# Optimization experiments

Hardware: AMD Instinct MI355X
Metric: run time of the kernel (lower is better)

## Reference

```python
import jax, jax.numpy as jnp
import numpy as np

B, DIM, H, W = 8, 384, 64, 64
HEADS = 8
D = DIM // HEADS          # 48
D2 = D // 2               # 24
DU = D // 3 * 2           # 32 (ratio=3)


def setup_inputs() -> dict:
    key = jax.random.key(0)
    ks = jax.random.split(key, 12)
    s = lambda k, shape, scale=0.05: jax.random.normal(k, shape, jnp.float32) * scale
    return {
        "x": jax.random.normal(ks[0], (B, DIM, H, W), jnp.float32),
        "temperature": jnp.ones((HEADS, 1, 1), jnp.float32),
        "w_qkv": s(ks[1], (3 * DIM, DIM)),          # 1x1 conv, no bias
        "w_dw": s(ks[2], (3 * DIM, 1, 3, 3)),       # depthwise 3x3, groups=3*dim
        "w_proj": s(ks[3], (DIM, HEADS)),           # project_out 1x1
        "w_attn_r": s(ks[4], (1, D)),
        "w_v_r": s(ks[5], (D2, D)),
        "w_up1": s(ks[6], (DU, D2)),
        "b_up1": jnp.zeros((DU,), jnp.float32),
        "ln_w": jnp.ones((DU, HEADS, 1), jnp.float32),
        "ln_b": jnp.zeros((DU, HEADS, 1), jnp.float32),
        "w_up2": s(ks[7], (D, DU)),
        "b_up2": jnp.zeros((D,), jnp.float32),
        "w_attn_l": s(ks[8], (D2, D)),
        "w_v_l": s(ks[9], (D2, D)),
    }


def _qkv_attn(x, temperature, w_qkv, w_dw):
    # shared: qkv 1x1 conv -> depthwise 3x3 -> split, normalize, elementwise attn+softmax
    b, c, h, w = x.shape
    qkv = jnp.einsum('bchw,oc->bohw', x, w_qkv)
    qkv = jax.lax.conv_general_dilated(
        qkv, w_dw, (1, 1), 'SAME', feature_group_count=3 * c,
        dimension_numbers=('NCHW', 'OIHW', 'NCHW'))
    q, k, v = jnp.split(qkv, 3, axis=1)
    rs = lambda t: t.reshape(b, HEADS, D, h * w)  # b (head d) h w -> b head d (hw)
    q, k, v = rs(q), rs(k), rs(v)
    qn = q / jnp.maximum(jnp.linalg.norm(q, axis=-1, keepdims=True), 1e-12)
    kn = k / jnp.maximum(jnp.linalg.norm(k, axis=-1, keepdims=True), 1e-12)
    attn = jax.nn.softmax(qn * kn * temperature, axis=-1)  # [b, head, d, s]
    return attn, v


def _forward(x, temperature, w_qkv, w_dw, w_proj, w_attn_r, w_v_r,
             w_up1, b_up1, ln_w, ln_b, w_up2, b_up2, w_attn_l, w_v_l):
    b, c, h, w = x.shape
    attn, v = _qkv_attn(x, temperature, w_qkv, w_dw)

    # ---- spatial_pool (channel gating) ----
    input_x = jnp.einsum('bhds,od->bhos', v, w_v_r)                 # conv_v_right: [b,head,d2,s]
    cm = jax.nn.softmax(jnp.einsum('bhds,d->bhs', attn, w_attn_r[0]), axis=-1)  # conv_attn_right + softmax
    ctx = jnp.einsum('bhs,bhjs->bhj', cm, input_x)                  # [b,head,d2]
    ctx = ctx.transpose(0, 2, 1)[..., None]                         # [b, d2, head, 1]
    u = jnp.einsum('bchl,oc->bohl', ctx, w_up1) + b_up1[None, :, None, None]  # [b, DU, head, 1]
    mu = u.mean(axis=(1, 2, 3), keepdims=True)
    var = u.var(axis=(1, 2, 3), keepdims=True)
    u = (u - mu) / jnp.sqrt(var + 1e-5) * ln_w[None] + ln_b[None]   # LayerNorm([DU, 8, 1])
    u = jax.nn.relu(u)
    u = jnp.einsum('bchl,oc->bohl', u, w_up2) + b_up2[None, :, None, None]    # [b, D, head, 1]
    mask_ch = jax.nn.sigmoid(u).reshape(b, c, 1, 1)                 # view(b, head*D, 1, 1)
    out_channel = x * mask_ch

    # ---- channel_pool (spatial gating) ----
    g = jnp.einsum('bhds,od->bhos', attn, w_attn_l)                 # conv_attn_left: [b,head,d2,s]
    avg = jax.nn.softmax(g.mean(axis=-1), axis=-1)                  # avg-pool over s, softmax over d2
    theta = jnp.einsum('bhds,od->bhos', v, w_v_l)                   # conv_v_left: [b,head,d2,s]
    ctx2 = jnp.einsum('bhd,bhds->bhs', avg, theta)                  # matmul: [b,head,s]
    mask_sp = jax.nn.sigmoid(ctx2).reshape(b, HEADS, h, w)
    mask_sp = jnp.einsum('bchw,oc->bohw', mask_sp, w_proj)          # project_out
    out_spatial = x * mask_sp

    return out_spatial + out_channel


def reference(x, temperature, w_qkv, w_dw, w_proj, w_attn_r, w_v_r,
              w_up1, b_up1, ln_w, ln_b, w_up2, b_up2, w_attn_l, w_v_l):
    return _forward(x, temperature, w_qkv, w_dw, w_proj, w_attn_r, w_v_r,
                    w_up1, b_up1, ln_w, ln_b, w_up2, b_up2, w_attn_l, w_v_l)
```

## Files before the change

### kernel.cpp

```cpp
#include <hip/hip_runtime.h>
#include <math.h>


#define S4096 4096
#define C384  384
#define OC    1152

typedef unsigned short bfraw;
typedef unsigned int   u32;
typedef __attribute__((ext_vector_type(8))) short bf16x8;
typedef __attribute__((ext_vector_type(4))) float f32x4;

typedef __attribute__((address_space(3))) unsigned int lds_u32;
typedef const __attribute__((address_space(1))) unsigned int glb_u32;
__device__ __forceinline__ void gll16(const void* g, void* l) {
    __builtin_amdgcn_global_load_lds((glb_u32*)g, (lds_u32*)l, 16, 0, 0);
}

__device__ __forceinline__ bfraw f2bf(float f) {
    union { float f; u32 u; } c; c.f = f;
    u32 r = c.u + 0x7FFFu + ((c.u >> 16) & 1u);
    return (bfraw)(r >> 16);
}
__device__ __forceinline__ float bf2f(bfraw u) {
    union { u32 u; float f; } c; c.u = ((u32)u) << 16;
    return c.f;
}
__device__ __forceinline__ void unpack8(uint4 v, float* f) {
    f[0] = bf2f((bfraw)(v.x & 0xffff)); f[1] = bf2f((bfraw)(v.x >> 16));
    f[2] = bf2f((bfraw)(v.y & 0xffff)); f[3] = bf2f((bfraw)(v.y >> 16));
    f[4] = bf2f((bfraw)(v.z & 0xffff)); f[5] = bf2f((bfraw)(v.z >> 16));
    f[6] = bf2f((bfraw)(v.w & 0xffff)); f[7] = bf2f((bfraw)(v.w >> 16));
}
__device__ __forceinline__ uint4 pack8(const float* f) {
    union { bfraw us[8]; uint4 q; } p;
    #pragma unroll
    for (int i = 0; i < 8; i++) p.us[i] = f2bf(f[i]);
    return p.q;
}

__device__ __forceinline__ float blk_red(float v, float* s4, bool ismax) {
    #pragma unroll
    for (int off = 32; off; off >>= 1) {
        float o = __shfl_down(v, off, 64);
        v = ismax ? fmaxf(v, o) : (v + o);
    }
    __syncthreads();
    if ((threadIdx.x & 63) == 0) s4[threadIdx.x >> 6] = v;
    __syncthreads();
    return ismax ? fmaxf(fmaxf(s4[0], s4[1]), fmaxf(s4[2], s4[3]))
                 : ((s4[0] + s4[1]) + (s4[2] + s4[3]));
}

__global__ void k0_prep(const float* __restrict__ w_attn_l,
                        const float* __restrict__ w_v_l,
                        float* __restrict__ weff) {
    __shared__ float avg[24];
    const int tid = threadIdx.x;
    if (tid < 24) {
        float a = 0.f;
        for (int d = 0; d < 48; d++) a += w_attn_l[tid * 48 + d];
        avg[tid] = a * (1.f / 4096.f);
    }
    __syncthreads();
    if (tid == 0) {
        float M = -3.402823466e+38f;
        for (int o = 0; o < 24; o++) M = fmaxf(M, avg[o]);
        float S = 0.f;
        for (int o = 0; o < 24; o++) { avg[o] = __expf(avg[o] - M); S += avg[o]; }
        float inv = 1.f / S;
        for (int o = 0; o < 24; o++) avg[o] *= inv;
    }
    __syncthreads();
    if (tid < 48) {
        float a = 0.f;
        for (int o = 0; o < 24; o++) a += avg[o] * w_v_l[o * 48 + tid];
        weff[tid] = a;
    }
}

__global__ __launch_bounds__(256) void kA_prep(
    const float* __restrict__ w_qkv, bfraw* __restrict__ wF) {
    const int id = blockIdx.x * 256 + threadIdx.x;
    const int ob = id / 768, rem = id % 768;
    const int c = rem / 48, kb = rem % 48;
    const float* src = w_qkv + (size_t)(ob * 16 + c) * C384 + kb * 8;
    float f[8];
    *(float4*)f       = *(const float4*)src;
    *(float4*)(f + 4) = *(const float4*)(src + 4);
    *(uint4*)&wF[((size_t)(ob * 48 + kb) * 16 + c) * 8] = pack8(f);
}

__global__ __launch_bounds__(256) void kB_tr(
    const float* __restrict__ x, bfraw* __restrict__ xF, int b0) {
    const int cb = blockIdx.x, sb = blockIdx.y, bl = blockIdx.z;
    const int c0 = cb * 16, s0 = sb * 256;
    const int tid = threadIdx.x;
    __shared__ alignas(16) bfraw lt[16][264];
    {
        const int r = tid >> 4, seg = tid & 15;
        const float* src = x + ((size_t)(b0 + bl) * C384 + c0 + r) * S4096 + s0 + seg * 16;
        float f[16];
        #pragma unroll
        for (int i = 0; i < 4; i++) *(float4*)(f + i * 4) = *(const float4*)(src + i * 4);
        *(uint4*)&lt[r][seg * 16]     = pack8(f);
        *(uint4*)&lt[r][seg * 16 + 8] = pack8(f + 8);
    }
    __syncthreads();
    const int sbl = tid >> 4, c = tid & 15;
    bfraw* xFb = xF + (size_t)bl * S4096 * C384;
    #pragma unroll
    for (int kbl = 0; kbl < 2; kbl++) {
        union { bfraw us[8]; uint4 q; } p;
        #pragma unroll
        for (int j = 0; j < 8; j++) p.us[j] = lt[kbl * 8 + j][sbl * 16 + c];
        const size_t idx = (((size_t)((s0 >> 4) + sbl) * 48) + (c0 >> 3) + kbl) * 128 + c * 8;
        *(uint4*)&xFb[idx] = p.q;
    }
}

__global__ __launch_bounds__(256) void k1_gemm(
    const bfraw* __restrict__ wF, const bfraw* __restrict__ xF,
    bfraw* __restrict__ pre, int b0) {
    __shared__ alignas(16) bfraw a_sm[4096];
    __shared__ alignas(16) bfraw b_sm[4096];
    const int tid = threadIdx.x;
    const int wave = tid >> 6, lane = tid & 63;
    const int sT = blockIdx.x, oT = blockIdx.y, bl = blockIdx.z;
    const bfraw* xFb = xF + (size_t)bl * S4096 * C384;

    f32x4 acc[4][4];
    #pragma unroll
    for (int m = 0; m < 4; m++)
        #pragma unroll
        for (int n = 0; n < 4; n++) acc[m][n] = (f32x4){0, 0, 0, 0};

    const int wr = (wave >> 1) * 4;
    const int wc = (wave & 1) * 4;

    for (int ks = 0; ks < 12; ks++) {
        const int kb0 = ks * 4;
        #pragma unroll
        for (int i = 0; i < 2; i++) {
            const int c = tid + i * 256;
            const int rb = c >> 6, oct = (c >> 4) & 3, row = c & 15;
            const bfraw* src = wF + ((size_t)((oT * 8 + rb) * 48 + kb0 + oct) * 16 + row) * 8;
            gll16(src, &a_sm[(size_t)c * 8]);
        }
        #pragma unroll
        for (int i = 0; i < 2; i++) {
            const int c = tid + i * 256;
            const int cb = c >> 6, oct = (c >> 4) & 3, col = c & 15;
            const bfraw* src = xFb + ((size_t)((sT * 8 + cb) * 48 + kb0 + oct) * 16 + col) * 8;
            gll16(src, &b_sm[(size_t)c * 8]);
        }
        __syncthreads();
        bf16x8 af[4], bq[4];
        #pragma unroll
        for (int m = 0; m < 4; m++) af[m] = *(const bf16x8*)&a_sm[((wr + m) * 64 + lane) * 8];
        #pragma unroll
        for (int n = 0; n < 4; n++) bq[n] = *(const bf16x8*)&b_sm[((wc + n) * 64 + lane) * 8];
        #pragma unroll
        for (int m = 0; m < 4; m++)
            #pragma unroll
            for (int n = 0; n < 4; n++)
                acc[m][n] = __builtin_amdgcn_mfma_f32_16x16x32_bf16(af[m], bq[n], acc[m][n], 0, 0, 0);
        __syncthreads();
    }
    bfraw* op = pre + (size_t)bl * OC * S4096;
    const int orow0 = oT * 128 + (wave >> 1) * 64 + (lane >> 4) * 4;
    const int scol0 = sT * 128 + (wave & 1) * 64 + (lane & 15);
    #pragma unroll
    for (int m = 0; m < 4; m++)
        #pragma unroll
        for (int n = 0; n < 4; n++)
            #pragma unroll
            for (int r = 0; r < 4; r++)
                op[(size_t)(orow0 + m * 16 + r) * S4096 + scol0 + n * 16] = f2bf(acc[m][n][r]);
}

__device__ __forceinline__ void stencil8(const bfraw* plane, const float* w9,
                                         int ypad, int k7, int x0, float* acc) {
    #pragma unroll
    for (int j = 0; j < 8; j++) acc[j] = 0.f;
    #pragma unroll
    for (int dy = 0; dy < 3; dy++) {
        uint4 rv = *(const uint4*)&plane[(ypad + dy) * 64 + x0];
        float r[8]; unpack8(rv, r);
        float lft = __shfl_up(r[7], 1);
        float rgt = __shfl_down(r[0], 1);
        if (k7 == 0) lft = 0.f;
        if (k7 == 7) rgt = 0.f;
        const float w0 = w9[dy*3], w1 = w9[dy*3+1], w2 = w9[dy*3+2];
        acc[0] += w0*lft + w1*r[0] + w2*r[1];
        #pragma unroll
        for (int j = 1; j < 7; j++) acc[j] += w0*r[j-1] + w1*r[j] + w2*r[j+1];
        acc[7] += w0*r[6] + w1*r[7] + w2*rgt;
    }
}

__global__ __launch_bounds__(256) void k2f(
    const bfraw* __restrict__ pre, const float* __restrict__ w_dw,
    const float* __restrict__ temperature,
    bfraw* __restrict__ av, int b0) {
    const int idx = blockIdx.x;
    const int bl  = blockIdx.y;
    const int h   = idx / 48;
    const int tid = threadIdx.x;
    __shared__ alignas(16) bfraw pl[3][66 * 64];
    __shared__ float s4[4];

    const size_t pbase = (size_t)bl * OC * S4096;
    #pragma unroll
    for (int p = 0; p < 3; p++) {
        const bfraw* src = pre + pbase + (size_t)(idx + p * C384) * S4096;
        uint4 a = *(const uint4*)&src[tid * 16];
        uint4 b = *(const uint4*)&src[tid * 16 + 8];
        int y = tid >> 2, xq = (tid & 3) * 16;
        *(uint4*)&pl[p][(y + 1) * 64 + xq]     = a;
        *(uint4*)&pl[p][(y + 1) * 64 + xq + 8] = b;
    }
    if (tid < 64) {
        #pragma unroll
        for (int p = 0; p < 3; p++) { pl[p][tid] = 0; pl[p][65 * 64 + tid] = 0; }
    }
    float wq[9], wk[9], wv[9];
    #pragma unroll
    for (int i = 0; i < 9; i++) {
        wq[i] = w_dw[idx * 9 + i];
        wk[i] = w_dw[(idx + C384) * 9 + i];
        wv[i] = w_dw[(idx + 768) * 9 + i];
    }
    __syncthreads();

    const int sid0 = tid,        y0 = sid0 >> 3, k70 = sid0 & 7, x00 = k70 * 8;
    const int sid1 = tid + 256,  y1 = sid1 >> 3, k71 = sid1 & 7, x01 = k71 * 8;
    float qo[16], ko[16], vo[16];
    stencil8(pl[0], wq, y0, k70, x00, qo);
    stencil8(pl[0], wq, y1, k71, x01, qo + 8);
    stencil8(pl[1], wk, y0, k70, x00, ko);
    stencil8(pl[1], wk, y1, k71, x01, ko + 8);
    stencil8(pl[2], wv, y0, k70, x00, vo);
    stencil8(pl[2], wv, y1, k71, x01, vo + 8);

    float sq = 0.f, sk = 0.f;
    #pragma unroll
    for (int i = 0; i < 16; i++) { sq += qo[i] * qo[i]; sk += ko[i] * ko[i]; }
    float Sq = blk_red(sq, s4, false);
    float Sk = blk_red(sk, s4, false);
    float scale = temperature[h] /
        (fmaxf(sqrtf(Sq), 1e-12f) * fmaxf(sqrtf(Sk), 1e-12f));
    float lm = -3.402823466e+38f;
    #pragma unroll
    for (int i = 0; i < 16; i++) { qo[i] = qo[i] * ko[i] * scale; lm = fmaxf(lm, qo[i]); }
    float M = blk_red(lm, s4, true);
    float ls = 0.f;
    #pragma unroll
    for (int i = 0; i < 16; i++) { qo[i] = __expf(qo[i] - M); ls += qo[i]; }
    float Z = blk_red(ls, s4, false);
    float invZ = 1.f / Z;
    #pragma unroll
    for (int i = 0; i < 16; i++) qo[i] *= invZ;

    bfraw* adst = av + ((size_t)bl * 768 + idx) * S4096;
    bfraw* vdst = av + ((size_t)bl * 768 + 384 + idx) * S4096;
    *(uint4*)&adst[y0 * 64 + x00] = pack8(qo);
    *(uint4*)&adst[y1 * 64 + x01] = pack8(qo + 8);
    *(uint4*)&vdst[y0 * 64 + x00] = pack8(vo);
    *(uint4*)&vdst[y1 * 64 + x01] = pack8(vo + 8);
}

__global__ __launch_bounds__(256) void k4a(
    const bfraw* __restrict__ av, const float* __restrict__ w_attn_r,
    const float* __restrict__ weff,
    float* __restrict__ cmraw, float* __restrict__ c2raw, int b0) {
    const int h = blockIdx.x, bl = blockIdx.y, st = blockIdx.z;
    const int b = b0 + bl;
    const int tid = threadIdx.x;
    __shared__ float swr[48], swf[48];
    if (tid < 48) { swr[tid] = w_attn_r[tid]; swf[tid] = weff[tid]; }
    __syncthreads();
    const int s_off = st * 1024 + tid * 4;
    const bfraw* abase = av + ((size_t)bl * 768 + h * 48) * S4096 + s_off;
    const bfraw* vbase = abase + (size_t)384 * S4096;
    float cmr[4] = {0,0,0,0}, c2[4] = {0,0,0,0};
    for (int d = 0; d < 48; d++) {
        uint2 ua = *(const uint2*)(abase + (size_t)d * S4096);
        uint2 uv = *(const uint2*)(vbase + (size_t)d * S4096);
        const float wr = swr[d], wf = swf[d];
        cmr[0] += bf2f((bfraw)(ua.x & 0xffff)) * wr;
        cmr[1] += bf2f((bfraw)(ua.x >> 16))    * wr;
        cmr[2] += bf2f((bfraw)(ua.y & 0xffff)) * wr;
        cmr[3] += bf2f((bfraw)(ua.y >> 16))    * wr;
        c2[0]  += bf2f((bfraw)(uv.x & 0xffff)) * wf;
        c2[1]  += bf2f((bfraw)(uv.x >> 16))    * wf;
        c2[2]  += bf2f((bfraw)(uv.y & 0xffff)) * wf;
        c2[3]  += bf2f((bfraw)(uv.y >> 16))    * wf;
    }
    const size_t o = ((size_t)(b * 8 + h)) * S4096 + s_off;
    float4 a4 = {cmr[0], cmr[1], cmr[2], cmr[3]};
    float4 b4 = {c2[0], c2[1], c2[2], c2[3]};
    *(float4*)(cmraw + o) = a4;
    *(float4*)(c2raw + o) = b4;
}

__global__ __launch_bounds__(256) void k4b(
    const float* __restrict__ cmraw, const float* __restrict__ c2raw,
    bfraw* __restrict__ cmb, float* __restrict__ msp, int b0) {
    const int h = blockIdx.x, bl = blockIdx.y, b = b0 + bl;
    const int tid = threadIdx.x;
    __shared__ float s4[4];
    const size_t base = ((size_t)(b * 8 + h)) * S4096 + tid * 16;
    float v[16];
    #pragma unroll
    for (int i = 0; i < 4; i++) *(float4*)(v + i * 4) = *(const float4*)(cmraw + base + i * 4);
    float lm = -3.402823466e+38f;
    #pragma unroll
    for (int i = 0; i < 16; i++) lm = fmaxf(lm, v[i]);
    float M = blk_red(lm, s4, true);
    float ls = 0.f;
    #pragma unroll
    for (int i = 0; i < 16; i++) { v[i] = __expf(v[i] - M); ls += v[i]; }
    float Z = blk_red(ls, s4, false);
    float inv = 1.f / Z;
    #pragma unroll
    for (int i = 0; i < 16; i++) v[i] *= inv;
    *(uint4*)(cmb + base)     = pack8(v);
    *(uint4*)(cmb + base + 8) = pack8(v + 8);
    #pragma unroll
    for (int i = 0; i < 4; i++) {
        float4 c = *(const float4*)(c2raw + base + i * 4);
        float4 m;
        m.x = 1.f / (1.f + __expf(-c.x)); m.y = 1.f / (1.f + __expf(-c.y));
        m.z = 1.f / (1.f + __expf(-c.z)); m.w = 1.f / (1.f + __expf(-c.w));
        *(float4*)(msp + base + i * 4) = m;
    }
}

__global__ __launch_bounds__(256) void k5_vc(
    const bfraw* __restrict__ av, const bfraw* __restrict__ cmb,
    float* __restrict__ vc, int b0) {
    const int idx = blockIdx.x;
    const int bl = blockIdx.y, b = b0 + bl;
    const int h = idx / 48;
    const int tid = threadIdx.x;
    const bfraw* vr = av + ((size_t)bl * 768 + 384 + idx) * S4096 + tid * 16;
    const bfraw* cr = cmb + ((size_t)(b * 8 + h)) * S4096 + tid * 16;
    float vv[16], cc[16];
    { uint4 a = *(const uint4*)vr, c = *(const uint4*)(vr + 8); unpack8(a, vv); unpack8(c, vv + 8); }
    { uint4 a = *(const uint4*)cr, c = *(const uint4*)(cr + 8); unpack8(a, cc); unpack8(c, cc + 8); }
    float a = 0.f;
    #pragma unroll
    for (int i = 0; i < 16; i++) a += vv[i] * cc[i];
    __shared__ float s4[4];
    float S = blk_red(a, s4, false);
    if (tid == 0) vc[b * C384 + idx] = S;
}

__global__ __launch_bounds__(256) void k6_gate(
    const float* __restrict__ vc, const float* __restrict__ w_v_r,
    const float* __restrict__ w_up1, const float* __restrict__ b_up1,
    const float* __restrict__ ln_w, const float* __restrict__ ln_b,
    const float* __restrict__ w_up2, const float* __restrict__ b_up2,
    float* __restrict__ mch, int b0) {
    const int b = b0 + blockIdx.x;
    const int tid = threadIdx.x;
    __shared__ float s_vc[384], s_ctx[192], s_u[256], s4[4];
    for (int i = tid; i < 384; i += 256) s_vc[i] = vc[b * C384 + i];
    __syncthreads();
    if (tid < 192) {
        int hh = tid / 24, o = tid % 24;
        float a = 0.f;
        for (int d = 0; d < 48; d++) a += w_v_r[o * 48 + d] * s_vc[hh * 48 + d];
        s_ctx[hh * 24 + o] = a;
    }
    __syncthreads();
    float uval;
    {
        int o = tid >> 3, hh = tid & 7;
        float a = b_up1[o];
        for (int c = 0; c < 24; c++) a += w_up1[o * 24 + c] * s_ctx[hh * 24 + c];
        uval = a;
    }
    float mu  = blk_red(uval, s4, false) * (1.f / 256.f);
    float dv  = uval - mu;
    float var = blk_red(dv * dv, s4, false) * (1.f / 256.f);
    float un  = dv * rsqrtf(var + 1e-5f) * ln_w[tid] + ln_b[tid];
    s_u[tid] = fmaxf(un, 0.f);
    __syncthreads();
    for (int t = tid; t < 384; t += 256) {
        int o2 = t >> 3, hh = t & 7;
        float a = b_up2[o2];
        for (int o = 0; o < 32; o++) a += w_up2[o2 * 32 + o] * s_u[o * 8 + hh];
        mch[b * C384 + t] = 1.f / (1.f + __expf(-a));
    }
}

__global__ __launch_bounds__(256) void k7_out(
    const float* __restrict__ x, const float* __restrict__ w_proj,
    const float* __restrict__ mch, const float* __restrict__ msp,
    float* __restrict__ out, int b0) {
    const int st = blockIdx.x, cg = blockIdx.y, bl = blockIdx.z;
    const int b = b0 + bl;
    const int tid = threadIdx.x;
    const int s0 = st * 256, c0 = cg * 48;
    __shared__ float s_msp[8][256];
    __shared__ float s_mch[48];
    __shared__ float s_wp[48][8];
    for (int i = tid; i < 2048; i += 256) {
        int hh = i >> 8, ss = i & 255;
        s_msp[hh][ss] = msp[((size_t)(b * 8 + hh)) * S4096 + s0 + ss];
    }
    if (tid < 48) s_mch[tid] = mch[b * C384 + c0 + tid];
    for (int i = tid; i < 384; i += 256)
        s_wp[i >> 3][i & 7] = w_proj[(size_t)(c0 + (i >> 3)) * 8 + (i & 7)];
    __syncthreads();

    const int cl = tid >> 6;
    const int s4i = (tid & 63) * 4;
    float4 m[8];
    #pragma unroll
    for (int hh = 0; hh < 8; hh++) m[hh] = *(const float4*)&s_msp[hh][s4i];

    #pragma unroll 4
    for (int j = 0; j < 12; j++) {
        const int cloc = j * 4 + cl;
        const int c = c0 + cloc;
        const float base = s_mch[cloc];
        float4 a = {base, base, base, base};
        #pragma unroll
        for (int hh = 0; hh < 8; hh++) {
            const float wp = s_wp[cloc][hh];
            a.x += wp * m[hh].x; a.y += wp * m[hh].y;
            a.z += wp * m[hh].z; a.w += wp * m[hh].w;
        }
        const size_t o = ((size_t)b * C384 + c) * S4096 + s0 + s4i;
        float4 xv = *(const float4*)(x + o);
        a.x *= xv.x; a.y *= xv.y; a.z *= xv.z; a.w *= xv.w;
        *(float4*)(out + o) = a;
    }
}

extern "C" void kernel_launch(void* const* d_in, const int* in_sizes, int n_in,
                              void* d_out, int out_size, void* d_ws, size_t ws_size,
                              hipStream_t stream) {
    const float* x        = (const float*)d_in[0];
    const float* temp     = (const float*)d_in[1];
    const float* w_qkv    = (const float*)d_in[2];
    const float* w_dw     = (const float*)d_in[3];
    const float* w_proj   = (const float*)d_in[4];
    const float* w_attn_r = (const float*)d_in[5];
    const float* w_v_r    = (const float*)d_in[6];
    const float* w_up1    = (const float*)d_in[7];
    const float* b_up1    = (const float*)d_in[8];
    const float* ln_w     = (const float*)d_in[9];
    const float* ln_b     = (const float*)d_in[10];
    const float* w_up2    = (const float*)d_in[11];
    const float* b_up2    = (const float*)d_in[12];
    const float* w_attn_l = (const float*)d_in[13];
    const float* w_v_l    = (const float*)d_in[14];
    float* out = (float*)d_out;
    char* ws = (char*)d_ws;

    size_t off = 0;
    auto alloc = [&](size_t bytes) {
        size_t o = off; off = (off + bytes + 255) & ~(size_t)255; return o;
    };
    float* cmraw = (float*)(ws + alloc((size_t)64 * S4096 * 4));
    float* c2raw = (float*)(ws + alloc((size_t)64 * S4096 * 4));
    bfraw* cmb   = (bfraw*)(ws + alloc((size_t)64 * S4096 * 2));
    float* msp   = (float*)(ws + alloc((size_t)64 * S4096 * 4));
    float* vc    = (float*)(ws + alloc(3072 * 4));
    float* mch   = (float*)(ws + alloc(3072 * 4));
    float* weff  = (float*)(ws + alloc(256));
    bfraw* wF    = (bfraw*)(ws + alloc((size_t)55296 * 16));
    const size_t big_xF  = (size_t)S4096 * C384 * 2;
    const size_t big_pre = (size_t)OC * S4096 * 2;
    const size_t big_av  = (size_t)768 * S4096 * 2;
    int nb = (ws_size >= off + 8 * (big_xF + big_pre + big_av)) ? 8 : 1;
    bfraw* xF  = (bfraw*)(ws + alloc((size_t)nb * big_xF));
    bfraw* pre = (bfraw*)(ws + alloc((size_t)nb * big_pre));
    bfraw* av  = (bfraw*)(ws + alloc((size_t)nb * big_av));

    k0_prep<<<1, 64, 0, stream>>>(w_attn_l, w_v_l, weff);
    kA_prep<<<216, 256, 0, stream>>>(w_qkv, wF);
    for (int b0 = 0; b0 < 8; b0 += nb) {
        kB_tr<<<dim3(24, 16, nb), 256, 0, stream>>>(x, xF, b0);
        k1_gemm<<<dim3(32, 9, nb), 256, 0, stream>>>(wF, xF, pre, b0);
        k2f<<<dim3(384, nb), 256, 0, stream>>>(pre, w_dw, temp, av, b0);
        k4a<<<dim3(8, nb, 4), 256, 0, stream>>>(av, w_attn_r, weff, cmraw, c2raw, b0);
        k4b<<<dim3(8, nb), 256, 0, stream>>>(cmraw, c2raw, cmb, msp, b0);
        k5_vc<<<dim3(384, nb), 256, 0, stream>>>(av, cmb, vc, b0);
        k6_gate<<<dim3(nb), 256, 0, stream>>>(vc, w_v_r, w_up1, b_up1,
                                              ln_w, ln_b, w_up2, b_up2, mch, b0);
        k7_out<<<dim3(16, 8, nb), 256, 0, stream>>>(x, w_proj, mch, msp, out, b0);
    }
}
```

Baseline: 130.4 us.

## Double-buffer GEMM LDS loads, stage epilogue through LDS, merge prep kernels

The QKV GEMM now double-buffers its LDS tiles, issuing the global-to-LDS loads for the next K step before running the MFMAs on the current one. The epilogue writes the bf16 tile into padded LDS and then stores 16-byte vectors per row instead of scattered 2-byte stores. The tiny weff prep kernel is folded into kA_prep as an extra block, saving one launch. The larger LDS footprint (about 34 KB per block) may cut occupancy.

```diff
diff --git a/kernel.cpp b/kernel.cpp
--- a/kernel.cpp
+++ b/kernel.cpp
@@ -52,35 +52,35 @@
                  : ((s4[0] + s4[1]) + (s4[2] + s4[3]));
 }
 
-__global__ void k0_prep(const float* __restrict__ w_attn_l,
-                        const float* __restrict__ w_v_l,
-                        float* __restrict__ weff) {
-    __shared__ float avg[24];
-    const int tid = threadIdx.x;
-    if (tid < 24) {
-        float a = 0.f;
-        for (int d = 0; d < 48; d++) a += w_attn_l[tid * 48 + d];
-        avg[tid] = a * (1.f / 4096.f);
-    }
-    __syncthreads();
-    if (tid == 0) {
-        float M = -3.402823466e+38f;
-        for (int o = 0; o < 24; o++) M = fmaxf(M, avg[o]);
-        float S = 0.f;
-        for (int o = 0; o < 24; o++) { avg[o] = __expf(avg[o] - M); S += avg[o]; }
-        float inv = 1.f / S;
-        for (int o = 0; o < 24; o++) avg[o] *= inv;
-    }
-    __syncthreads();
-    if (tid < 48) {
-        float a = 0.f;
-        for (int o = 0; o < 24; o++) a += avg[o] * w_v_l[o * 48 + tid];
-        weff[tid] = a;
-    }
-}
-
 __global__ __launch_bounds__(256) void kA_prep(
-    const float* __restrict__ w_qkv, bfraw* __restrict__ wF) {
+    const float* __restrict__ w_qkv, bfraw* __restrict__ wF,
+    const float* __restrict__ w_attn_l, const float* __restrict__ w_v_l,
+    float* __restrict__ weff) {
+    if (blockIdx.x == 216) {
+        __shared__ float avg[24];
+        const int tid = threadIdx.x;
+        if (tid < 24) {
+            float a = 0.f;
+            for (int d = 0; d < 48; d++) a += w_attn_l[tid * 48 + d];
+            avg[tid] = a * (1.f / 4096.f);
+        }
+        __syncthreads();
+        if (tid == 0) {
+            float M = -3.402823466e+38f;
+            for (int o = 0; o < 24; o++) M = fmaxf(M, avg[o]);
+            float S = 0.f;
+            for (int o = 0; o < 24; o++) { avg[o] = __expf(avg[o] - M); S += avg[o]; }
+            float inv = 1.f / S;
+            for (int o = 0; o < 24; o++) avg[o] *= inv;
+        }
+        __syncthreads();
+        if (tid < 48) {
+            float a = 0.f;
+            for (int o = 0; o < 24; o++) a += avg[o] * w_v_l[o * 48 + tid];
+            weff[tid] = a;
+        }
+        return;
+    }
     const int id = blockIdx.x * 256 + threadIdx.x;
     const int ob = id / 768, rem = id % 768;
     const int c = rem / 48, kb = rem % 48;
@@ -122,13 +122,16 @@
 __global__ __launch_bounds__(256) void k1_gemm(
     const bfraw* __restrict__ wF, const bfraw* __restrict__ xF,
     bfraw* __restrict__ pre, int b0) {
-    __shared__ alignas(16) bfraw a_sm[4096];
-    __shared__ alignas(16) bfraw b_sm[4096];
+    __shared__ alignas(16) bfraw smem[17408];
     const int tid = threadIdx.x;
     const int wave = tid >> 6, lane = tid & 63;
     const int sT = blockIdx.x, oT = blockIdx.y, bl = blockIdx.z;
     const bfraw* xFb = xF + (size_t)bl * S4096 * C384;
 
+    const int c0_ = tid, c1_ = tid + 256;
+    const int rb0 = c0_ >> 6, oc0 = (c0_ >> 4) & 3, rw0 = c0_ & 15;
+    const int rb1 = c1_ >> 6, oc1 = (c1_ >> 4) & 3, rw1 = c1_ & 15;
+
     f32x4 acc[4][4];
     #pragma unroll
     for (int m = 0; m < 4; m++)
@@ -138,28 +141,30 @@
     const int wr = (wave >> 1) * 4;
     const int wc = (wave & 1) * 4;
 
+    auto stage = [&](bfraw* dst, int kb0) {
+        gll16(wF  + ((size_t)((oT * 8 + rb0) * 48 + kb0 + oc0) * 16 + rw0) * 8,
+              dst + (size_t)c0_ * 8);
+        gll16(wF  + ((size_t)((oT * 8 + rb1) * 48 + kb0 + oc1) * 16 + rw1) * 8,
+              dst + (size_t)c1_ * 8);
+        gll16(xFb + ((size_t)((sT * 8 + rb0) * 48 + kb0 + oc0) * 16 + rw0) * 8,
+              dst + 4096 + (size_t)c0_ * 8);
+        gll16(xFb + ((size_t)((sT * 8 + rb1) * 48 + kb0 + oc1) * 16 + rw1) * 8,
+              dst + 4096 + (size_t)c1_ * 8);
+    };
+
+    stage(smem, 0);
+    __syncthreads();
+
     for (int ks = 0; ks < 12; ks++) {
-        const int kb0 = ks * 4;
-        #pragma unroll
-        for (int i = 0; i < 2; i++) {
-            const int c = tid + i * 256;
-            const int rb = c >> 6, oct = (c >> 4) & 3, row = c & 15;
-            const bfraw* src = wF + ((size_t)((oT * 8 + rb) * 48 + kb0 + oct) * 16 + row) * 8;
-            gll16(src, &a_sm[(size_t)c * 8]);
-        }
-        #pragma unroll
-        for (int i = 0; i < 2; i++) {
-            const int c = tid + i * 256;
-            const int cb = c >> 6, oct = (c >> 4) & 3, col = c & 15;
-            const bfraw* src = xFb + ((size_t)((sT * 8 + cb) * 48 + kb0 + oct) * 16 + col) * 8;
-            gll16(src, &b_sm[(size_t)c * 8]);
-        }
-        __syncthreads();
+        bfraw* cb = smem + (size_t)(ks & 1) * 8192;
         bf16x8 af[4], bq[4];
         #pragma unroll
-        for (int m = 0; m < 4; m++) af[m] = *(const bf16x8*)&a_sm[((wr + m) * 64 + lane) * 8];
-        #pragma unroll
-        for (int n = 0; n < 4; n++) bq[n] = *(const bf16x8*)&b_sm[((wc + n) * 64 + lane) * 8];
+        for (int m = 0; m < 4; m++)
+            af[m] = *(const bf16x8*)&cb[((wr + m) * 64 + lane) * 8];
+        #pragma unroll
+        for (int n = 0; n < 4; n++)
+            bq[n] = *(const bf16x8*)&cb[4096 + ((wc + n) * 64 + lane) * 8];
+        if (ks < 11) stage(smem + (size_t)((ks & 1) ^ 1) * 8192, (ks + 1) * 4);
         #pragma unroll
         for (int m = 0; m < 4; m++)
             #pragma unroll
@@ -167,16 +172,24 @@
                 acc[m][n] = __builtin_amdgcn_mfma_f32_16x16x32_bf16(af[m], bq[n], acc[m][n], 0, 0, 0);
         __syncthreads();
     }
-    bfraw* op = pre + (size_t)bl * OC * S4096;
-    const int orow0 = oT * 128 + (wave >> 1) * 64 + (lane >> 4) * 4;
-    const int scol0 = sT * 128 + (wave & 1) * 64 + (lane & 15);
+
+    const int er0 = (wave >> 1) * 64 + (lane >> 4) * 4;
+    const int ec0 = (wave & 1) * 64 + (lane & 15);
     #pragma unroll
     for (int m = 0; m < 4; m++)
         #pragma unroll
         for (int n = 0; n < 4; n++)
             #pragma unroll
             for (int r = 0; r < 4; r++)
-                op[(size_t)(orow0 + m * 16 + r) * S4096 + scol0 + n * 16] = f2bf(acc[m][n][r]);
+                smem[(er0 + m * 16 + r) * 136 + ec0 + n * 16] = f2bf(acc[m][n][r]);
+    __syncthreads();
+    const int row = tid >> 1, hh = tid & 1;
+    bfraw* op = pre + (size_t)bl * OC * S4096
+              + (size_t)(oT * 128 + row) * S4096 + sT * 128 + hh * 8;
+    const bfraw* es = &smem[row * 136 + hh * 8];
+    #pragma unroll
+    for (int j = 0; j < 8; j++)
+        *(uint4*)(op + j * 16) = *(const uint4*)(es + j * 16);
 }
 
 __device__ __forceinline__ void stencil8(const bfraw* plane, const float* w9,
@@ -482,8 +495,7 @@
     bfraw* pre = (bfraw*)(ws + alloc((size_t)nb * big_pre));
     bfraw* av  = (bfraw*)(ws + alloc((size_t)nb * big_av));
 
-    k0_prep<<<1, 64, 0, stream>>>(w_attn_l, w_v_l, weff);
-    kA_prep<<<216, 256, 0, stream>>>(w_qkv, wF);
+    kA_prep<<<217, 256, 0, stream>>>(w_qkv, wF, w_attn_l, w_v_l, weff);
     for (int b0 = 0; b0 < 8; b0 += nb) {
         kB_tr<<<dim3(24, 16, nb), 256, 0, stream>>>(x, xF, b0);
         k1_gemm<<<dim3(32, 9, nb), 256, 0, stream>>>(wF, xF, pre, b0);
```

After: 128.0 us. Within noise of the previous version (-1.8%).
